# Performance work log

Hardware: AMD Instinct MI355X
Metric: run time of the kernel (lower is better)

## Reference

```python
import jax, jax.numpy as jnp
import numpy as np

B, N, M, D = 64, 16384, 64, 512
EPS = 1e-16


def setup_inputs() -> dict:
    key = jax.random.key(0)
    k1, k2, k3, k4 = jax.random.split(key, 4)
    controller_output = jax.random.normal(k1, (B, D), dtype=jnp.float32)
    w_prev = jax.random.uniform(k2, (B, N), dtype=jnp.float32)
    memory = jax.random.normal(k3, (B, N, M), dtype=jnp.float32)
    W = jax.random.normal(k4, (M + 6, D), dtype=jnp.float32) * (1.0 / np.sqrt(D))
    b = jnp.zeros((M + 6,), dtype=jnp.float32)
    return {"controller_output": controller_output, "w_prev": w_prev,
            "memory": memory, "W": W, "b": b}


def reference(controller_output, w_prev, memory, W, b):
    # fc_read projection -> [B, M+6], split into k, beta, g, s, gamma
    o = controller_output @ W.T + b
    k = o[:, :M]                      # [B, M] content key
    beta = jax.nn.softplus(o[:, M:M + 1])        # [B, 1] key strength
    g = jax.nn.sigmoid(o[:, M + 1:M + 2])        # [B, 1] interpolation gate
    s = jax.nn.softmax(o[:, M + 2:M + 5], axis=1)  # [B, 3] shift weights
    gamma = 1.0 + jax.nn.softplus(o[:, M + 5:M + 6])  # [B, 1] sharpening

    # content addressing: cosine similarity between k and each memory row
    num = jnp.einsum('bm,bnm->bn', k, memory)                      # [B, N]
    denom = (jnp.linalg.norm(k, axis=1, keepdims=True)
             * jnp.linalg.norm(memory, axis=2) + EPS)              # [B, N]
    w_c = jax.nn.softmax(beta * (num / denom), axis=1)             # [B, N]

    # interpolation with previous weighting
    w_g = g * w_c + (1.0 - g) * w_prev                              # [B, N]

    # circular convolution shift over {-1, 0, +1}
    w_t = (s[:, 0:1] * jnp.roll(w_g, 1, axis=1)
           + s[:, 1:2] * w_g
           + s[:, 2:3] * jnp.roll(w_g, -1, axis=1))                 # [B, N]

    # sharpening
    w_pow = w_t ** gamma
    w = w_pow / (jnp.sum(w_pow, axis=1, keepdims=True) + EPS)       # [B, N]

    # read: weighted sum of memory rows
    r = jnp.einsum('bn,bnm->bm', w, memory)                         # [B, M]
    return (r, w)
```

## Files before the change

### kernel.cpp

```cpp
#include <hip/hip_runtime.h>
#include <math.h>

#define B 64
#define N 16384
#define MDIM 64
#define DDIM 512
#define EPSF 1e-16f

#define K_OFF      0
#define SCAL_OFF   (B*64)
#define SCORE_OFF  (SCAL_OFF + B*8)
#define MS_OFF     (SCORE_OFF + B*N)
#define MXI_OFF    (MS_OFF + B*64)
#define PSUM_OFF   (MXI_OFF + B*2)
#define INVP_OFF   (PSUM_OFF + B*32)
#define PART_OFF   (INVP_OFF + B)

__device__ __forceinline__ float rowsum16(float x) {
    float t;
    t = __int_as_float(__builtin_amdgcn_update_dpp(0, __float_as_int(x), 0x128, 0xF, 0xF, true)); x += t;
    t = __int_as_float(__builtin_amdgcn_update_dpp(0, __float_as_int(x), 0x124, 0xF, 0xF, true)); x += t;
    t = __int_as_float(__builtin_amdgcn_update_dpp(0, __float_as_int(x), 0x122, 0xF, 0xF, true)); x += t;
    t = __int_as_float(__builtin_amdgcn_update_dpp(0, __float_as_int(x), 0x121, 0xF, 0xF, true)); x += t;
    return x;
}

__global__ __launch_bounds__(256) void k1(const float* __restrict__ c,
                                          const float* __restrict__ W,
                                          const float* __restrict__ bias,
                                          float* __restrict__ ws) {
    int b = blockIdx.x;
    __shared__ float cs[DDIM];
    __shared__ float osh[72];
    int tid = threadIdx.x;
    for (int i = tid; i < DDIM; i += 256) cs[i] = c[b * DDIM + i];
    __syncthreads();
    int wave = tid >> 6, lane = tid & 63;
    for (int j = wave; j < MDIM + 6; j += 4) {
        const float* wr = W + (size_t)j * DDIM;
        float sum = 0.f;
        for (int d = lane; d < DDIM; d += 64) sum += cs[d] * wr[d];
        for (int off = 32; off > 0; off >>= 1) sum += __shfl_xor(sum, off);
        if (lane == 0) osh[j] = sum + bias[j];
    }
    __syncthreads();
    if (tid < 64) ws[K_OFF + b * 64 + tid] = osh[tid];
    if (wave == 0) {
        float v = osh[lane];
        float sq = v * v;
        for (int off = 32; off > 0; off >>= 1) sq += __shfl_xor(sq, off);
        if (lane == 0) {
            float kn = sqrtf(sq);
            float ob = osh[64], og = osh[65], os0 = osh[66], os1 = osh[67],
                  os2 = osh[68], ogm = osh[69];
            float beta  = fmaxf(ob, 0.f) + log1pf(expf(-fabsf(ob)));
            float g     = 1.f / (1.f + expf(-og));
            float mx    = fmaxf(os0, fmaxf(os1, os2));
            float e0 = expf(os0 - mx), e1 = expf(os1 - mx), e2 = expf(os2 - mx);
            float es = e0 + e1 + e2;
            float gamma = 1.f + fmaxf(ogm, 0.f) + log1pf(expf(-fabsf(ogm)));
            float* sc = ws + SCAL_OFF + b * 8;
            sc[0] = kn; sc[1] = beta; sc[2] = g;
            sc[3] = e0 / es; sc[4] = e1 / es; sc[5] = e2 / es;
            sc[6] = gamma;
        }
    }
}

__global__ __launch_bounds__(256) void k2(const float* __restrict__ mem,
                                          float* __restrict__ ws) {
    int b = blockIdx.x >> 5, chunk = blockIdx.x & 31;
    __shared__ float ks[64];
    __shared__ float kb2[2];
    __shared__ float scbuf[512];
    int tid = threadIdx.x;
    if (tid < 64) ks[tid] = ws[K_OFF + b * 64 + tid];
    if (tid == 64) kb2[0] = ws[SCAL_OFF + b * 8 + 0];
    if (tid == 65) kb2[1] = ws[SCAL_OFF + b * 8 + 1];
    __syncthreads();
    float kn = kb2[0], beta = kb2[1];
    int grp = tid >> 4, ll = tid & 15;
    float k0 = ks[ll * 4], k1v = ks[ll * 4 + 1], k2v = ks[ll * 4 + 2], k3v = ks[ll * 4 + 3];
    int row0 = chunk * 512;
    #pragma unroll 8
    for (int it = 0; it < 32; ++it) {
        int lrow = it * 16 + grp;
        int row = row0 + lrow;
        float4 v = *reinterpret_cast<const float4*>(
            mem + ((size_t)b * N + row) * MDIM + ll * 4);
        float dot = v.x * k0 + v.y * k1v + v.z * k2v + v.w * k3v;
        float sq  = v.x * v.x + v.y * v.y + v.z * v.z + v.w * v.w;
        dot = rowsum16(dot);
        sq  = rowsum16(sq);
        if (ll == 0) {
            float score = beta * (dot / (kn * sqrtf(sq) + EPSF));
            ws[SCORE_OFF + (size_t)b * N + row] = score;
            scbuf[lrow] = score;
        }
    }
    __syncthreads();
    if (tid < 64) {
        float vr[8];
        float m = -1e30f;
        #pragma unroll
        for (int j = 0; j < 8; ++j) {
            vr[j] = scbuf[tid + 64 * j];
            m = fmaxf(m, vr[j]);
        }
        #pragma unroll
        for (int off = 32; off > 0; off >>= 1) m = fmaxf(m, __shfl_xor(m, off));
        float s = 0.f;
        #pragma unroll
        for (int j = 0; j < 8; ++j) s += __expf(vr[j] - m);
        #pragma unroll
        for (int off = 32; off > 0; off >>= 1) s += __shfl_xor(s, off);
        if (tid == 0) {
            ws[MS_OFF + ((size_t)b * 32 + chunk) * 2]     = m;
            ws[MS_OFF + ((size_t)b * 32 + chunk) * 2 + 1] = s;
        }
    }
}

__global__ __launch_bounds__(64) void kc(float* __restrict__ ws) {
    int b = blockIdx.x, lane = threadIdx.x;
    float m = -1e30f, s = 0.f;
    if (lane < 32) {
        m = ws[MS_OFF + ((size_t)b * 32 + lane) * 2];
        s = ws[MS_OFF + ((size_t)b * 32 + lane) * 2 + 1];
    }
    #pragma unroll
    for (int off = 32; off > 0; off >>= 1) {
        float m2 = __shfl_xor(m, off), s2 = __shfl_xor(s, off);
        float M = fmaxf(m, m2);
        s = s * __expf(m - M) + s2 * __expf(m2 - M);
        m = M;
    }
    if (lane == 0) {
        ws[MXI_OFF + b * 2]     = m;
        ws[MXI_OFF + b * 2 + 1] = 1.f / s;
    }
}

__global__ __launch_bounds__(256) void krw(const float* __restrict__ mem,
                                           const float* __restrict__ w_prev,
                                           float* __restrict__ ws,
                                           float* __restrict__ w_out,
                                           float* __restrict__ part) {
    int b = blockIdx.x >> 5, chunk = blockIdx.x & 31;
    int tid = threadIdx.x, wave = tid >> 6, lane = tid & 63;
    __shared__ float wgL[514];
    __shared__ float wpl[512];
    __shared__ float lds[16][64];
    __shared__ float red[4];
    const float* sl = ws + SCAL_OFF + b * 8;
    float g = sl[2], s0 = sl[3], s1 = sl[4], s2 = sl[5], gamma = sl[6];
    float mx  = ws[MXI_OFF + b * 2];
    float inv = ws[MXI_OFF + b * 2 + 1];
    const float* sc = ws + SCORE_OFF + (size_t)b * N;
    const float* wp = w_prev + (size_t)b * N;
    int row0 = chunk * 512;

    {
        int r0 = row0 + tid;
        wgL[tid + 1]   = g * (__expf(sc[r0] - mx) * inv) + (1.f - g) * wp[r0];
        int r1 = row0 + tid + 256;
        wgL[tid + 257] = g * (__expf(sc[r1] - mx) * inv) + (1.f - g) * wp[r1];
        if (tid == 0) {
            int rl = (row0 - 1) & (N - 1);
            wgL[0] = g * (__expf(sc[rl] - mx) * inv) + (1.f - g) * wp[rl];
        }
        if (tid == 255) {
            int rr = (row0 + 512) & (N - 1);
            wgL[513] = g * (__expf(sc[rr] - mx) * inv) + (1.f - g) * wp[rr];
        }
    }
    __syncthreads();

    float wt0 = s0 * wgL[tid]       + s1 * wgL[tid + 1]   + s2 * wgL[tid + 2];
    float wt1 = s0 * wgL[tid + 256] + s1 * wgL[tid + 257] + s2 * wgL[tid + 258];
    float p0 = __expf(gamma * __logf(wt0));
    float p1 = __expf(gamma * __logf(wt1));
    wpl[tid] = p0;
    wpl[tid + 256] = p1;
    float* wo = w_out + (size_t)b * N + row0;
    wo[tid]       = p0;
    wo[tid + 256] = p1;

    float sp = p0 + p1;
    #pragma unroll
    for (int off = 32; off > 0; off >>= 1) sp += __shfl_xor(sp, off);
    if (lane == 0) red[wave] = sp;
    __syncthreads();
    if (tid == 0)
        ws[PSUM_OFF + b * 32 + chunk] = red[0] + red[1] + red[2] + red[3];

    int grp = tid >> 4, ll = tid & 15;
    float4 acc = make_float4(0.f, 0.f, 0.f, 0.f);
    #pragma unroll 8
    for (int it = 0; it < 32; ++it) {
        int lrow = it * 16 + grp;
        float wv = wpl[lrow];
        float4 v = *reinterpret_cast<const float4*>(
            mem + ((size_t)b * N + row0 + lrow) * MDIM + ll * 4);
        acc.x += wv * v.x; acc.y += wv * v.y; acc.z += wv * v.z; acc.w += wv * v.w;
    }
    lds[grp][ll * 4 + 0] = acc.x;
    lds[grp][ll * 4 + 1] = acc.y;
    lds[grp][ll * 4 + 2] = acc.z;
    lds[grp][ll * 4 + 3] = acc.w;
    __syncthreads();
    if (tid < 64) {
        float sacc = 0.f;
        #pragma unroll
        for (int gi = 0; gi < 16; ++gi) sacc += lds[gi][tid];
        part[(size_t)blockIdx.x * 64 + tid] = sacc;
    }
}

__global__ __launch_bounds__(64) void krr(const float* __restrict__ part,
                                          float* __restrict__ ws,
                                          float* __restrict__ r) {
    int b = blockIdx.x, tid = threadIdx.x;
    float s = (tid < 32) ? ws[PSUM_OFF + b * 32 + tid] : 0.f;
    #pragma unroll
    for (int off = 32; off > 0; off >>= 1) s += __shfl_xor(s, off);
    float invp = 1.f / (s + EPSF);
    if (tid == 0) ws[INVP_OFF + b] = invp;
    float srr = 0.f;
    #pragma unroll
    for (int c = 0; c < 32; ++c) srr += part[((size_t)b * 32 + c) * 64 + tid];
    r[b * 64 + tid] = srr * invp;
}

__global__ __launch_bounds__(256) void kwf(const float* __restrict__ ws,
                                           float* __restrict__ w_out) {
    int b = blockIdx.x >> 5, chunk = blockIdx.x & 31;
    int tid = threadIdx.x;
    float invp = ws[INVP_OFF + b];
    size_t base = (size_t)b * N + chunk * 512;
    w_out[base + tid]       *= invp;
    w_out[base + tid + 256] *= invp;
}

extern "C" void kernel_launch(void* const* d_in, const int* in_sizes, int n_in,
                              void* d_out, int out_size, void* d_ws, size_t ws_size,
                              hipStream_t stream) {
    const float* c      = (const float*)d_in[0];
    const float* w_prev = (const float*)d_in[1];
    const float* mem    = (const float*)d_in[2];
    const float* W      = (const float*)d_in[3];
    const float* bias   = (const float*)d_in[4];
    float* out = (float*)d_out;
    float* r_out = out;
    float* w_out = out + B * MDIM;
    float* ws = (float*)d_ws;

    k1 <<<B,      256, 0, stream>>>(c, W, bias, ws);
    k2 <<<B * 32, 256, 0, stream>>>(mem, ws);
    kc <<<B,       64, 0, stream>>>(ws);
    krw<<<B * 32, 256, 0, stream>>>(mem, w_prev, ws, w_out, ws + PART_OFF);
    krr<<<B,       64, 0, stream>>>(ws + PART_OFF, ws, r_out);
    kwf<<<B * 32, 256, 0, stream>>>(ws, w_out);
}
```

Baseline: 111.9 us.

## Fold tiny reduction kernels into neighbors and coalesce score writes

```diff
diff --git a/kernel.cpp b/kernel.cpp
--- a/kernel.cpp
+++ b/kernel.cpp
@@ -6,15 +6,16 @@
 #define MDIM 64
 #define DDIM 512
 #define EPSF 1e-16f
+#define NCH 32
+#define CHUNK 512
+#define GRID (B * NCH)
 
 #define K_OFF      0
 #define SCAL_OFF   (B*64)
 #define SCORE_OFF  (SCAL_OFF + B*8)
 #define MS_OFF     (SCORE_OFF + B*N)
-#define MXI_OFF    (MS_OFF + B*64)
-#define PSUM_OFF   (MXI_OFF + B*2)
-#define INVP_OFF   (PSUM_OFF + B*32)
-#define PART_OFF   (INVP_OFF + B)
+#define PSUM_OFF   (MS_OFF + B*NCH*2)
+#define PART_OFF   (PSUM_OFF + B*NCH)
 
 __device__ __forceinline__ float rowsum16(float x) {
     float t;
@@ -72,7 +73,7 @@
     int b = blockIdx.x >> 5, chunk = blockIdx.x & 31;
     __shared__ float ks[64];
     __shared__ float kb2[2];
-    __shared__ float scbuf[512];
+    __shared__ float scbuf[CHUNK];
     int tid = threadIdx.x;
     if (tid < 64) ks[tid] = ws[K_OFF + b * 64 + tid];
     if (tid == 64) kb2[0] = ws[SCAL_OFF + b * 8 + 0];
@@ -81,24 +82,26 @@
     float kn = kb2[0], beta = kb2[1];
     int grp = tid >> 4, ll = tid & 15;
     float k0 = ks[ll * 4], k1v = ks[ll * 4 + 1], k2v = ks[ll * 4 + 2], k3v = ks[ll * 4 + 3];
-    int row0 = chunk * 512;
+    int row0 = chunk * CHUNK;
     #pragma unroll 8
-    for (int it = 0; it < 32; ++it) {
+    for (int it = 0; it < CHUNK / 16; ++it) {
         int lrow = it * 16 + grp;
-        int row = row0 + lrow;
         float4 v = *reinterpret_cast<const float4*>(
-            mem + ((size_t)b * N + row) * MDIM + ll * 4);
+            mem + ((size_t)b * N + row0 + lrow) * MDIM + ll * 4);
         float dot = v.x * k0 + v.y * k1v + v.z * k2v + v.w * k3v;
         float sq  = v.x * v.x + v.y * v.y + v.z * v.z + v.w * v.w;
         dot = rowsum16(dot);
         sq  = rowsum16(sq);
-        if (ll == 0) {
-            float score = beta * (dot / (kn * sqrtf(sq) + EPSF));
-            ws[SCORE_OFF + (size_t)b * N + row] = score;
-            scbuf[lrow] = score;
-        }
-    }
-    __syncthreads();
+        if (ll == 0)
+            scbuf[lrow] = beta * (dot / (kn * sqrtf(sq) + EPSF));
+    }
+    __syncthreads();
+    {
+        float s0v = scbuf[tid], s1v = scbuf[tid + 256];
+        float* sco = ws + SCORE_OFF + (size_t)b * N + row0;
+        sco[tid] = s0v;
+        sco[tid + 256] = s1v;
+    }
     if (tid < 64) {
         float vr[8];
         float m = -1e30f;
@@ -115,29 +118,9 @@
         #pragma unroll
         for (int off = 32; off > 0; off >>= 1) s += __shfl_xor(s, off);
         if (tid == 0) {
-            ws[MS_OFF + ((size_t)b * 32 + chunk) * 2]     = m;
-            ws[MS_OFF + ((size_t)b * 32 + chunk) * 2 + 1] = s;
-        }
-    }
-}
-
-__global__ __launch_bounds__(64) void kc(float* __restrict__ ws) {
-    int b = blockIdx.x, lane = threadIdx.x;
-    float m = -1e30f, s = 0.f;
-    if (lane < 32) {
-        m = ws[MS_OFF + ((size_t)b * 32 + lane) * 2];
-        s = ws[MS_OFF + ((size_t)b * 32 + lane) * 2 + 1];
-    }
-    #pragma unroll
-    for (int off = 32; off > 0; off >>= 1) {
-        float m2 = __shfl_xor(m, off), s2 = __shfl_xor(s, off);
-        float M = fmaxf(m, m2);
-        s = s * __expf(m - M) + s2 * __expf(m2 - M);
-        m = M;
-    }
-    if (lane == 0) {
-        ws[MXI_OFF + b * 2]     = m;
-        ws[MXI_OFF + b * 2 + 1] = 1.f / s;
+            ws[MS_OFF + ((size_t)b * NCH + chunk) * 2]     = m;
+            ws[MS_OFF + ((size_t)b * NCH + chunk) * 2 + 1] = s;
+        }
     }
 }
 
@@ -148,17 +131,27 @@
                                            float* __restrict__ part) {
     int b = blockIdx.x >> 5, chunk = blockIdx.x & 31;
     int tid = threadIdx.x, wave = tid >> 6, lane = tid & 63;
-    __shared__ float wgL[514];
-    __shared__ float wpl[512];
+    __shared__ float wgL[CHUNK + 2];
+    __shared__ float wpl[CHUNK];
     __shared__ float lds[16][64];
     __shared__ float red[4];
     const float* sl = ws + SCAL_OFF + b * 8;
     float g = sl[2], s0 = sl[3], s1 = sl[4], s2 = sl[5], gamma = sl[6];
-    float mx  = ws[MXI_OFF + b * 2];
-    float inv = ws[MXI_OFF + b * 2 + 1];
+
+    float mx = -1e30f, ssum = 0.f;
+    const float* msp = ws + MS_OFF + (size_t)b * NCH * 2;
+    #pragma unroll
+    for (int i = 0; i < NCH; ++i) {
+        float mi = msp[i * 2], si = msp[i * 2 + 1];
+        float M = fmaxf(mx, mi);
+        ssum = ssum * __expf(mx - M) + si * __expf(mi - M);
+        mx = M;
+    }
+    float inv = 1.f / ssum;
+
     const float* sc = ws + SCORE_OFF + (size_t)b * N;
     const float* wp = w_prev + (size_t)b * N;
-    int row0 = chunk * 512;
+    int row0 = chunk * CHUNK;
 
     {
         int r0 = row0 + tid;
@@ -170,8 +163,8 @@
             wgL[0] = g * (__expf(sc[rl] - mx) * inv) + (1.f - g) * wp[rl];
         }
         if (tid == 255) {
-            int rr = (row0 + 512) & (N - 1);
-            wgL[513] = g * (__expf(sc[rr] - mx) * inv) + (1.f - g) * wp[rr];
+            int rr = (row0 + CHUNK) & (N - 1);
+            wgL[CHUNK + 1] = g * (__expf(sc[rr] - mx) * inv) + (1.f - g) * wp[rr];
         }
     }
     __syncthreads();
@@ -192,12 +185,12 @@
     if (lane == 0) red[wave] = sp;
     __syncthreads();
     if (tid == 0)
-        ws[PSUM_OFF + b * 32 + chunk] = red[0] + red[1] + red[2] + red[3];
+        ws[PSUM_OFF + (size_t)b * NCH + chunk] = red[0] + red[1] + red[2] + red[3];
 
     int grp = tid >> 4, ll = tid & 15;
     float4 acc = make_float4(0.f, 0.f, 0.f, 0.f);
     #pragma unroll 8
-    for (int it = 0; it < 32; ++it) {
+    for (int it = 0; it < CHUNK / 16; ++it) {
         int lrow = it * 16 + grp;
         float wv = wpl[lrow];
         float4 v = *reinterpret_cast<const float4*>(
@@ -217,29 +210,31 @@
     }
 }
 
-__global__ __launch_bounds__(64) void krr(const float* __restrict__ part,
-                                          float* __restrict__ ws,
-                                          float* __restrict__ r) {
-    int b = blockIdx.x, tid = threadIdx.x;
-    float s = (tid < 32) ? ws[PSUM_OFF + b * 32 + tid] : 0.f;
-    #pragma unroll
-    for (int off = 32; off > 0; off >>= 1) s += __shfl_xor(s, off);
-    float invp = 1.f / (s + EPSF);
-    if (tid == 0) ws[INVP_OFF + b] = invp;
-    float srr = 0.f;
-    #pragma unroll
-    for (int c = 0; c < 32; ++c) srr += part[((size_t)b * 32 + c) * 64 + tid];
-    r[b * 64 + tid] = srr * invp;
-}
-
-__global__ __launch_bounds__(256) void kwf(const float* __restrict__ ws,
-                                           float* __restrict__ w_out) {
+__global__ __launch_bounds__(256) void kfin(const float* __restrict__ part,
+                                            float* __restrict__ ws,
+                                            float* __restrict__ w_out,
+                                            float* __restrict__ r) {
     int b = blockIdx.x >> 5, chunk = blockIdx.x & 31;
     int tid = threadIdx.x;
-    float invp = ws[INVP_OFF + b];
-    size_t base = (size_t)b * N + chunk * 512;
+    __shared__ float invps;
+    if (tid < 64) {
+        float s = (tid < 32) ? ws[PSUM_OFF + (size_t)b * NCH + tid] : 0.f;
+        #pragma unroll
+        for (int off = 32; off > 0; off >>= 1) s += __shfl_xor(s, off);
+        if (tid == 0) invps = 1.f / (s + EPSF);
+    }
+    __syncthreads();
+    float invp = invps;
+    size_t base = (size_t)b * N + chunk * CHUNK;
     w_out[base + tid]       *= invp;
     w_out[base + tid + 256] *= invp;
+    if (chunk == 0 && tid < 64) {
+        float srr = 0.f;
+        #pragma unroll
+        for (int c2 = 0; c2 < NCH; ++c2)
+            srr += part[((size_t)b * NCH + c2) * 64 + tid];
+        r[b * 64 + tid] = srr * invp;
+    }
 }
 
 extern "C" void kernel_launch(void* const* d_in, const int* in_sizes, int n_in,
@@ -254,11 +249,10 @@
     float* r_out = out;
     float* w_out = out + B * MDIM;
     float* ws = (float*)d_ws;
-
-    k1 <<<B,      256, 0, stream>>>(c, W, bias, ws);
-    k2 <<<B * 32, 256, 0, stream>>>(mem, ws);
-    kc <<<B,       64, 0, stream>>>(ws);
-    krw<<<B * 32, 256, 0, stream>>>(mem, w_prev, ws, w_out, ws + PART_OFF);
-    krr<<<B,       64, 0, stream>>>(ws + PART_OFF, ws, r_out);
-    kwf<<<B * 32, 256, 0, stream>>>(ws, w_out);
-}
+    float* part = ws + PART_OFF;
+
+    k1  <<<B,    256, 0, stream>>>(c, W, bias, ws);
+    k2  <<<GRID, 256, 0, stream>>>(mem, ws);
+    krw <<<GRID, 256, 0, stream>>>(mem, w_prev, ws, w_out, part);
+    kfin<<<GRID, 256, 0, stream>>>(part, ws, w_out, r_out);
+}
```

Measured after the change: 111.0 us. No clear change (-0.8%).
